# Performance work log

Measured on AMD Instinct MI355X. Metric: run time of the kernel, lower is better.

## Reference

```python
import math
import jax, jax.numpy as jnp
import numpy as np

B, N, T, C, H = 16, 307, 24, 128, 8
D = C // H
FACTOR = 5
S = min(FACTOR * int(np.ceil(np.log(T))), T)   # sample_k (U_part) = 20
U = S                                          # n_top u = 20


def _pos_emb(t_len, c):
    pos = jnp.arange(t_len, dtype=jnp.float32)[:, None]
    div = jnp.exp(jnp.arange(0, c, 2, dtype=jnp.float32) * (-math.log(10000.0) / c))
    pe = jnp.zeros((t_len, c), dtype=jnp.float32)
    pe = pe.at[:, 0::2].set(jnp.sin(pos * div))
    pe = pe.at[:, 1::2].set(jnp.cos(pos * div))
    return pe  # [T, C]


def _layernorm(x, g, b, eps=1e-5):
    m = x.mean(-1, keepdims=True)
    v = ((x - m) ** 2).mean(-1, keepdims=True)
    return (x - m) / jnp.sqrt(v + eps) * g + b


def _forward(query, time_encoder, index_sample,
             emb_minute, emb_hour, emb_weekday, emb_month, emb_year,
             Wq, Wk, Wv, Wo, bo, ff_w1, ff_b1, ff_w2, ff_b2,
             ln1_g, ln1_b, ln2_g, ln2_b):
    # DataEmbedding: x + positional + temporal (dropout = identity in eval)
    pe = _pos_emb(T, C)                                   # [T, C]
    te = (emb_minute[time_encoder[..., 0]] + emb_hour[time_encoder[..., 1]]
          + emb_weekday[time_encoder[..., 2]] + emb_month[time_encoder[..., 3]]
          + emb_year[time_encoder[..., 4]])               # [B, T, C]
    x = query + pe[None, None, :, :] + te[:, None, :, :]  # [B, N, T, C]

    # QKV projections -> [B, H, N, T, D]
    def proj(inp, W):
        return (inp @ W).reshape(B, N, T, H, D).transpose(0, 3, 1, 2, 4)
    Q, K, V = proj(x, Wq), proj(x, Wk), proj(x, Wv)

    # ProbSparse: sample S keys per query position
    K_samp = K[:, :, :, index_sample, :]                  # [B, H, N, T, S, D]
    QK_samp = jnp.einsum('bhntd,bhntsd->bhnts', Q, K_samp)
    M = QK_samp.max(-1) - QK_samp.sum(-1) / S             # [B, H, N, T]
    _, M_top = jax.lax.top_k(M, U)                        # [B, H, N, U]

    Q_red = jnp.take_along_axis(Q, M_top[..., None], axis=3)  # [B, H, N, U, D]
    scores = jnp.einsum('bhnud,bhntd->bhnut', Q_red, K) * (1.0 / math.sqrt(D))
    attn = jax.nn.softmax(scores, axis=-1)
    upd = jnp.einsum('bhnut,bhntd->bhnud', attn, V)       # [B, H, N, U, D]

    # initial context = mean over T, then scatter-update top-u query rows
    ctx = jnp.broadcast_to(V.mean(axis=3, keepdims=True), V.shape)
    ctx = ctx.at[jnp.arange(B)[:, None, None, None],
                 jnp.arange(H)[None, :, None, None],
                 jnp.arange(N)[None, None, :, None],
                 M_top].set(upd)

    ctx = ctx.transpose(0, 2, 3, 1, 4).reshape(B, N, T, C)
    att_out = ctx @ Wo + bo

    x1 = _layernorm(att_out + x, ln1_g, ln1_b)
    ff = jax.nn.relu(x1 @ ff_w1 + ff_b1) @ ff_w2 + ff_b2
    out = _layernorm(ff + x1, ln2_g, ln2_b)
    return out


def setup_inputs() -> dict:
    key = jax.random.key(0)
    ks = jax.random.split(key, 32)
    def nrm(i, shape, s=0.02):
        return jax.random.normal(ks[i], shape, dtype=jnp.float32) * s
    inp = {
        'value': jax.random.normal(ks[0], (B, N, T, C), dtype=jnp.float32),
        'key_in': jax.random.normal(ks[1], (B, N, T, C), dtype=jnp.float32),
        'query': jax.random.normal(ks[2], (B, N, T, C), dtype=jnp.float32),
        't': 1,
        'time_encoder': jax.random.randint(ks[3], (B, T, 5), 0, 10),
        'index_sample': jax.random.randint(ks[4], (T, S), 0, T),
        'emb_minute': nrm(5, (70, C), 1.0), 'emb_hour': nrm(6, (30, C), 1.0),
        'emb_weekday': nrm(7, (10, C), 1.0), 'emb_month': nrm(8, (40, C), 1.0),
        'emb_year': nrm(9, (400, C), 1.0),
        'Wq': nrm(10, (C, C)), 'Wk': nrm(11, (C, C)), 'Wv': nrm(12, (C, C)),
        'Wo': nrm(13, (C, C)), 'bo': jnp.zeros((C,), jnp.float32),
        'ff_w1': nrm(14, (C, 4 * C)), 'ff_b1': jnp.zeros((4 * C,), jnp.float32),
        'ff_w2': nrm(15, (4 * C, C)), 'ff_b2': jnp.zeros((C,), jnp.float32),
        'ln1_g': jnp.ones((C,), jnp.float32), 'ln1_b': jnp.zeros((C,), jnp.float32),
        'ln2_g': jnp.ones((C,), jnp.float32), 'ln2_b': jnp.zeros((C,), jnp.float32),
    }
    return inp


def reference(value, key_in, query, t, time_encoder, index_sample,
              emb_minute, emb_hour, emb_weekday, emb_month, emb_year,
              Wq, Wk, Wv, Wo, bo, ff_w1, ff_b1, ff_w2, ff_b2,
              ln1_g, ln1_b, ln2_g, ln2_b):
    # value, key_in, t are accepted but unused, matching the torch module
    return _forward(query, time_encoder, index_sample,
                    emb_minute, emb_hour, emb_weekday, emb_month, emb_year,
                    Wq, Wk, Wv, Wo, bo, ff_w1, ff_b1, ff_w2, ff_b2,
                    ln1_g, ln1_b, ln2_g, ln2_b)
```

## Files before the change

### kernel.cpp

```cpp
#include <hip/hip_runtime.h>
#include <hip/hip_bf16.h>
#include <cmath>

namespace {
constexpr int B_ = 16, N_ = 307, T_ = 24, C_ = 128, H_ = 8, D_ = 16, S_ = 20, U_ = 20;
constexpr int NROW = B_ * N_ * T_;
constexpr int NX = NROW * C_;
constexpr int TEPE_N = B_ * T_ * C_;
constexpr int FF = 4 * C_;
constexpr int BM = 32;
constexpr int NBLK_MM = NROW / BM;
constexpr int BMF = 64;
constexpr int NBLK_FF = NROW / BMF;
constexpr int NUNIT = B_ * H_ * N_;
}

typedef __attribute__((ext_vector_type(8))) short short8;
typedef __attribute__((ext_vector_type(4))) short short4_;
typedef __attribute__((ext_vector_type(4))) float f32x4;

__device__ inline short f2bf(float v) {
    union { float f; unsigned u; } a; a.f = v;
    unsigned r = a.u + 0x7fff + ((a.u >> 16) & 1);
    return (short)(r >> 16);
}
__device__ inline float bf2f(short s) {
    return __bfloat162float(*(const __hip_bfloat16*)&s);
}

__global__ void k_tepe(const int* __restrict__ te,
                       const float* __restrict__ e_min, const float* __restrict__ e_hr,
                       const float* __restrict__ e_wd, const float* __restrict__ e_mo,
                       const float* __restrict__ e_yr, float* __restrict__ tepe,
                       const int* __restrict__ idxs, unsigned char* __restrict__ cntg) {
    int i = blockIdx.x * blockDim.x + threadIdx.x;
    if (i < TEPE_N) {
        int c = i & (C_ - 1);
        int bt = i >> 7;
        int t = bt % T_;
        const int* enc = te + bt * 5;
        float v = e_min[enc[0] * C_ + c] + e_hr[enc[1] * C_ + c] + e_wd[enc[2] * C_ + c]
                + e_mo[enc[3] * C_ + c] + e_yr[enc[4] * C_ + c];
        float ang = (float)t * expf(-(float)(c & ~1) * (9.210340371976184f / 128.0f));
        v += (c & 1) ? cosf(ang) : sinf(ang);
        tepe[i] = v;
    }
    if (blockIdx.x == 0) {
        __shared__ int scnt[T_ * 32];
        for (int j = threadIdx.x; j < T_ * 32; j += 256) scnt[j] = 0;
        __syncthreads();
        for (int j = threadIdx.x; j < T_ * S_; j += 256) {
            int t = j / S_;
            atomicAdd(&scnt[t * 32 + idxs[j]], 1);
        }
        __syncthreads();
        for (int j = threadIdx.x; j < 192; j += 256) {
            unsigned v = (unsigned)scnt[4 * j] | ((unsigned)scnt[4 * j + 1] << 8)
                       | ((unsigned)scnt[4 * j + 2] << 16) | ((unsigned)scnt[4 * j + 3] << 24);
            ((unsigned*)cntg)[j] = v;
        }
    }
}

__global__ void k_xprep(const float* __restrict__ query, const float* __restrict__ tepe,
                        short* __restrict__ xbf) {
    int i = blockIdx.x * 256 + threadIdx.x;
    int c4 = i & 31;
    int gr = i >> 5;
    int t = gr % T_;
    int b = gr / (N_ * T_);
    float4 q = *(const float4*)(query + 4 * (size_t)i);
    float4 p = *(const float4*)(tepe + (size_t)(b * T_ + t) * C_ + c4 * 4);
    short4_ s;
    s.x = f2bf(q.x + p.x); s.y = f2bf(q.y + p.y);
    s.z = f2bf(q.z + p.z); s.w = f2bf(q.w + p.w);
    *(short4_*)&xbf[4 * (size_t)i] = s;
}

__global__ void k_wcvt_qkv(const float* __restrict__ Wq, const float* __restrict__ Wk,
                           const float* __restrict__ Wv, short* __restrict__ wqkvf) {
    int i = blockIdx.x * 256 + threadIdx.x;
    int tile = i >> 9, l = (i >> 3) & 63, e = i & 7;
    int c_tile = tile >> 2, ks = tile & 3;
    int c_all = c_tile * 16 + (l & 15);
    int k = ks * 32 + (l >> 4) * 8 + e;
    int m = c_all >> 7, c = c_all & (C_ - 1);
    const float* W = (m == 0) ? Wq : (m == 1) ? Wk : Wv;
    wqkvf[i] = f2bf(W[k * C_ + c]);
}

__global__ void k_wcvt2(const float* __restrict__ w1, const float* __restrict__ w2,
                        const float* __restrict__ Wo,
                        short* __restrict__ w1f, short* __restrict__ w2f,
                        short* __restrict__ wof) {
    int i = blockIdx.x * 256 + threadIdx.x;
    if (i < C_ * FF) {
        int tile = i >> 9, l = (i >> 3) & 63, e = i & 7;
        int jtile = tile >> 2, ks = tile & 3;
        int j = jtile * 16 + (l & 15);
        int k = ks * 32 + (l >> 4) * 8 + e;
        w1f[i] = f2bf(w1[k * FF + j]);
    } else if (i < 2 * C_ * FF) {
        int i2 = i - C_ * FF;
        int tile = i2 >> 9, l = (i2 >> 3) & 63, e = i2 & 7;
        int c_tile = tile >> 4, ks = tile & 15;
        int c = c_tile * 16 + (l & 15);
        int j = ks * 32 + (l >> 4) * 8 + e;
        w2f[i2] = f2bf(w2[j * C_ + c]);
    } else {
        int i3 = i - 2 * C_ * FF;
        int tile = i3 >> 9, l = (i3 >> 3) & 63, e = i3 & 7;
        int c_tile = tile >> 2, ks = tile & 3;
        int c = c_tile * 16 + (l & 15);
        int k = ks * 32 + (l >> 4) * 8 + e;
        wof[i3] = f2bf(Wo[k * C_ + c]);
    }
}

__global__ __launch_bounds__(256) void k_qkv_mfma(
    const short* __restrict__ xbf, const short* __restrict__ wqkvf,
    short* __restrict__ Q, short* __restrict__ K, short* __restrict__ V) {
    __shared__ __align__(16) short xs[BM * C_];
    int tid = threadIdx.x;
    int r0 = blockIdx.x * BM;
    {
        int row = tid >> 3;
        int cb = (tid & 7) * 16;
        const short* src = xbf + (size_t)(r0 + row) * C_ + cb;
        short8 v0 = *(const short8*)(src);
        short8 v1 = *(const short8*)(src + 8);
        *(short8*)&xs[(row * C_ + cb) ^ ((row & 7) << 3)] = v0;
        *(short8*)&xs[(row * C_ + cb + 8) ^ ((row & 7) << 3)] = v1;
    }
    __syncthreads();
    int w = tid >> 6, l = tid & 63;
    int lr = l & 15, lk = l >> 4;
    int swz = (lr & 7) << 3;
    short8 bx[2][4];
#pragma unroll
    for (int rt = 0; rt < 2; rt++)
#pragma unroll
        for (int ks = 0; ks < 4; ks++)
            bx[rt][ks] = *(const short8*)&xs[((rt * 16 + lr) * C_ + ks * 32 + lk * 8) ^ swz];
    size_t base[2];
#pragma unroll
    for (int rt = 0; rt < 2; rt++) {
        int gr = r0 + rt * 16 + lr;
        int t = gr % T_;
        int n = (gr / T_) % N_;
        int b = gr / (N_ * T_);
        base[rt] = ((size_t)b * H_ * N_ + n) * (T_ * D_) + t * D_;
    }
#pragma unroll
    for (int jt = 0; jt < 6; jt++) {
        int ctile = w * 6 + jt;
        const short* ap = wqkvf + (size_t)ctile * 2048 + l * 8;
        short8 acur[4];
#pragma unroll
        for (int ks = 0; ks < 4; ks++) acur[ks] = *(const short8*)(ap + ks * 512);
        f32x4 acc[2] = {{0.f, 0.f, 0.f, 0.f}, {0.f, 0.f, 0.f, 0.f}};
#pragma unroll
        for (int ks = 0; ks < 4; ks++) {
#pragma unroll
            for (int rt = 0; rt < 2; rt++)
                acc[rt] = __builtin_amdgcn_mfma_f32_16x16x32_bf16(acur[ks], bx[rt][ks], acc[rt], 0, 0, 0);
        }
        int c0 = ctile * 16 + lk * 4;
        int m = c0 >> 7;
        int c = c0 & (C_ - 1);
        int h = c >> 4, d = c & 15;
        short* dst = (m == 0) ? Q : (m == 1) ? K : V;
#pragma unroll
        for (int rt = 0; rt < 2; rt++) {
            short4_ sv;
            sv.x = f2bf(acc[rt][0]); sv.y = f2bf(acc[rt][1]);
            sv.z = f2bf(acc[rt][2]); sv.w = f2bf(acc[rt][3]);
            *(short4_*)&dst[base[rt] + (size_t)h * (N_ * T_ * D_) + d] = sv;
        }
    }
}

__global__ __launch_bounds__(256) void k_attn(
    const short* __restrict__ Q, const short* __restrict__ K, const short* __restrict__ V,
    const unsigned char* __restrict__ cntg, short* __restrict__ ctx) {
    __shared__ __align__(16) short Qbf[4][32 * 24], Kbf[4][32 * 24];
    __shared__ __align__(16) short Vt[4][16 * 40];
    __shared__ __align__(16) short Pbf[4][32 * 40];
    __shared__ unsigned char cntS[T_ * 32];
    __shared__ float Mv[4][T_];
    __shared__ int keepS[4][T_];
    __shared__ float meanVs[4][D_];
    int tid = threadIdx.x;
    int wid = tid >> 6, l = tid & 63;
    int e = blockIdx.x * 4 + wid;
    const short* qb = Q + (size_t)e * (T_ * D_);
    const short* kb = K + (size_t)e * (T_ * D_);
    const short* vb = V + (size_t)e * (T_ * D_);
    if (l < 48) {
        int t = l >> 1, hf = l & 1;
        *(short8*)&Qbf[wid][t * 24 + hf * 8] = *(const short8*)(qb + t * 16 + hf * 8);
        *(short8*)&Kbf[wid][t * 24 + hf * 8] = *(const short8*)(kb + t * 16 + hf * 8);
    }
    for (int i = l; i < 96; i += 64) {
        int t = i >> 2, c4 = i & 3;
        short4_ v = *(const short4_*)(vb + t * 16 + c4 * 4);
        Vt[wid][(c4 * 4 + 0) * 40 + t] = v.x;
        Vt[wid][(c4 * 4 + 1) * 40 + t] = v.y;
        Vt[wid][(c4 * 4 + 2) * 40 + t] = v.z;
        Vt[wid][(c4 * 4 + 3) * 40 + t] = v.w;
    }
    for (int i = l; i < 128; i += 64) {
        int d = i >> 3, c = 24 + (i & 7);
        Vt[wid][d * 40 + c] = 0;
    }
    if (tid < 192) ((int*)cntS)[tid] = ((const int*)cntg)[tid];
    __syncthreads();
    if (l >= 48) {
        int d = l - 48;
        float s = 0.f;
        for (int t = 0; t < T_; t++) s += bf2f(Vt[wid][d * 40 + t]);
        meanVs[wid][d] = s * (1.0f / T_);
    }
    int lr = l & 15, lk = l >> 4;
    short8 zz = {};
    short8 kf0 = zz, kf1 = zz, qf0 = zz, qf1 = zz;
    if (lk < 2) {
        kf0 = *(const short8*)&Kbf[wid][lr * 24 + lk * 8];
        kf1 = *(const short8*)&Kbf[wid][(16 + lr) * 24 + lk * 8];
        qf0 = *(const short8*)&Qbf[wid][lr * 24 + lk * 8];
        qf1 = *(const short8*)&Qbf[wid][(16 + lr) * 24 + lk * 8];
    }
    f32x4 zf = {0.f, 0.f, 0.f, 0.f};
    f32x4 s00 = __builtin_amdgcn_mfma_f32_16x16x32_bf16(kf0, qf0, zf, 0, 0, 0);
    f32x4 s01 = __builtin_amdgcn_mfma_f32_16x16x32_bf16(kf1, qf0, zf, 0, 0, 0);
    f32x4 s10 = __builtin_amdgcn_mfma_f32_16x16x32_bf16(kf0, qf1, zf, 0, 0, 0);
    f32x4 s11 = __builtin_amdgcn_mfma_f32_16x16x32_bf16(kf1, qf1, zf, 0, 0, 0);
#pragma unroll
    for (int rt = 0; rt < 2; rt++) {
        int t = rt * 16 + lr;
        int tt = (t < T_) ? t : 0;
        f32x4 c0 = rt ? s10 : s00;
        f32x4 c1 = rt ? s11 : s01;
        float mx = -1e30f, sm = 0.f;
#pragma unroll
        for (int i = 0; i < 4; i++) {
            int cA = cntS[tt * 32 + lk * 4 + i];
            if (cA) { mx = fmaxf(mx, c0[i]); sm += (float)cA * c0[i]; }
        }
        if (lk < 2) {
#pragma unroll
            for (int i = 0; i < 4; i++) {
                int cB = cntS[tt * 32 + 16 + lk * 4 + i];
                if (cB) { mx = fmaxf(mx, c1[i]); sm += (float)cB * c1[i]; }
            }
        }
        mx = fmaxf(mx, __shfl_xor(mx, 16));
        mx = fmaxf(mx, __shfl_xor(mx, 32));
        sm += __shfl_xor(sm, 16);
        sm += __shfl_xor(sm, 32);
        if (lk == 0 && t < T_) Mv[wid][t] = mx - sm * (1.0f / S_);
    }
    __syncthreads();
    if (l < T_) {
        float mt = Mv[wid][l];
        int cnt2 = 0;
        for (int t2 = 0; t2 < T_; t2++) {
            float m2 = Mv[wid][t2];
            cnt2 += (m2 > mt) || (m2 == mt && t2 < l);
        }
        keepS[wid][l] = (cnt2 < U_) ? 1 : 0;
    }
#pragma unroll
    for (int rt = 0; rt < 2; rt++) {
        f32x4 c0 = rt ? s10 : s00;
        f32x4 c1 = rt ? s11 : s01;
        float lm = fmaxf(fmaxf(c0[0], c0[1]), fmaxf(c0[2], c0[3]));
        if (lk < 2) lm = fmaxf(lm, fmaxf(fmaxf(c1[0], c1[1]), fmaxf(c1[2], c1[3])));
        lm = fmaxf(lm, __shfl_xor(lm, 16));
        lm = fmaxf(lm, __shfl_xor(lm, 32));
        float e0[4], e1[4];
        float ls = 0.f;
#pragma unroll
        for (int i = 0; i < 4; i++) { e0[i] = __expf(0.25f * (c0[i] - lm)); ls += e0[i]; }
#pragma unroll
        for (int i = 0; i < 4; i++) { e1[i] = (lk < 2) ? __expf(0.25f * (c1[i] - lm)) : 0.f; ls += e1[i]; }
        ls += __shfl_xor(ls, 16);
        ls += __shfl_xor(ls, 32);
        float inv = 1.0f / ls;
        short4_ w0, w1;
        w0.x = f2bf(e0[0] * inv); w0.y = f2bf(e0[1] * inv);
        w0.z = f2bf(e0[2] * inv); w0.w = f2bf(e0[3] * inv);
        w1.x = f2bf(e1[0] * inv); w1.y = f2bf(e1[1] * inv);
        w1.z = f2bf(e1[2] * inv); w1.w = f2bf(e1[3] * inv);
        int trow = rt * 16 + lr;
        *(short4_*)&Pbf[wid][trow * 40 + lk * 4] = w0;
        *(short4_*)&Pbf[wid][trow * 40 + 16 + lk * 4] = w1;
    }
    __syncthreads();
    short8 vf = *(const short8*)&Vt[wid][lr * 40 + lk * 8];
    short8 pf0 = *(const short8*)&Pbf[wid][lr * 40 + lk * 8];
    short8 pf1 = *(const short8*)&Pbf[wid][(16 + lr) * 40 + lk * 8];
    f32x4 u0 = __builtin_amdgcn_mfma_f32_16x16x32_bf16(vf, pf0, zf, 0, 0, 0);
    f32x4 u1 = __builtin_amdgcn_mfma_f32_16x16x32_bf16(vf, pf1, zf, 0, 0, 0);
    int b = e / (H_ * N_);
    int h = (e / N_) % H_;
    int n = e % N_;
    float4 mv4 = *(const float4*)&meanVs[wid][lk * 4];
#pragma unroll
    for (int rt = 0; rt < 2; rt++) {
        int t = rt * 16 + lr;
        if (t < T_) {
            f32x4 u = rt ? u1 : u0;
            float4 o;
            if (keepS[wid][t]) { o.x = u[0]; o.y = u[1]; o.z = u[2]; o.w = u[3]; }
            else o = mv4;
            short4_ sv;
            sv.x = f2bf(o.x); sv.y = f2bf(o.y); sv.z = f2bf(o.z); sv.w = f2bf(o.w);
            *(short4_*)&ctx[((size_t)(b * N_ + n) * T_ + t) * C_ + h * D_ + lk * 4] = sv;
        }
    }
}

__global__ __launch_bounds__(256) void k_out_ln_mfma(
    const short* __restrict__ ctx, const short* __restrict__ wof, const float* __restrict__ bo,
    const float* __restrict__ query, const float* __restrict__ tepe,
    const float* __restrict__ g1, const float* __restrict__ b1,
    float* __restrict__ x1) {
    __shared__ __align__(16) short cbf[BM * C_];
    __shared__ __align__(16) float xf[BM][132];
    int tid = threadIdx.x;
    int r0 = blockIdx.x * BM;
    {
        int row = tid >> 3;
        int cb = (tid & 7) * 16;
        int gr = r0 + row;
        int t = gr % T_;
        int b = gr / (N_ * T_);
        const short* src = ctx + (size_t)gr * C_ + cb;
        const float* qsrc = query + (size_t)gr * C_ + cb;
        const float* tsrc = tepe + (size_t)(b * T_ + t) * C_ + cb;
        short8 v0 = *(const short8*)(src);
        short8 v1 = *(const short8*)(src + 8);
        int swz0 = (row & 7) << 3;
        *(short8*)&cbf[(row * C_ + cb) ^ swz0] = v0;
        *(short8*)&cbf[(row * C_ + cb + 8) ^ swz0] = v1;
#pragma unroll
        for (int i = 0; i < 4; i++) {
            float4 q4 = *(const float4*)(qsrc + 4 * i);
            float4 t4 = *(const float4*)(tsrc + 4 * i);
            float4 xr;
            xr.x = q4.x + t4.x; xr.y = q4.y + t4.y;
            xr.z = q4.z + t4.z; xr.w = q4.w + t4.w;
            *(float4*)&xf[row][cb + 4 * i] = xr;
        }
    }
    __syncthreads();
    int w = tid >> 6, l = tid & 63;
    int lr = l & 15, lk = l >> 4;
    int swz = (lr & 7) << 3;
    short8 bc[2][4];
#pragma unroll
    for (int rt = 0; rt < 2; rt++)
#pragma unroll
        for (int ks = 0; ks < 4; ks++)
            bc[rt][ks] = *(const short8*)&cbf[((rt * 16 + lr) * C_ + ks * 32 + lk * 8) ^ swz];
#pragma unroll
    for (int ct = 0; ct < 2; ct++) {
        int c_tile = w * 2 + ct;
        const short* ap = wof + (size_t)c_tile * 2048 + l * 8;
        short8 acur[4];
#pragma unroll
        for (int ks = 0; ks < 4; ks++) acur[ks] = *(const short8*)(ap + ks * 512);
        f32x4 acc[2] = {{0.f, 0.f, 0.f, 0.f}, {0.f, 0.f, 0.f, 0.f}};
#pragma unroll
        for (int ks = 0; ks < 4; ks++) {
#pragma unroll
            for (int rt = 0; rt < 2; rt++)
                acc[rt] = __builtin_amdgcn_mfma_f32_16x16x32_bf16(acur[ks], bc[rt][ks], acc[rt], 0, 0, 0);
        }
        int cc = c_tile * 16 + lk * 4;
        float4 bias = *(const float4*)(bo + cc);
#pragma unroll
        for (int rt = 0; rt < 2; rt++) {
            int rrow = rt * 16 + lr;
            float4 res = *(const float4*)&xf[rrow][cc];
            float4 o;
            o.x = acc[rt][0] + bias.x + res.x;
            o.y = acc[rt][1] + bias.y + res.y;
            o.z = acc[rt][2] + bias.z + res.z;
            o.w = acc[rt][3] + bias.w + res.w;
            *(float4*)&xf[rrow][cc] = o;
        }
    }
    __syncthreads();
    {
        int r = tid >> 3;
        int q = tid & 7;
        int cb = q * 16;
        float vals[16];
        float s = 0.f;
#pragma unroll
        for (int i = 0; i < 16; i++) { vals[i] = xf[r][cb + i]; s += vals[i]; }
        s += __shfl_xor(s, 1, 8);
        s += __shfl_xor(s, 2, 8);
        s += __shfl_xor(s, 4, 8);
        float mean = s * (1.f / C_);
        float vv = 0.f;
#pragma unroll
        for (int i = 0; i < 16; i++) { float d = vals[i] - mean; vv += d * d; }
        vv += __shfl_xor(vv, 1, 8);
        vv += __shfl_xor(vv, 2, 8);
        vv += __shfl_xor(vv, 4, 8);
        float rstd = rsqrtf(vv * (1.f / C_) + 1e-5f);
        float* op = x1 + (size_t)(r0 + r) * C_ + cb;
#pragma unroll
        for (int i4 = 0; i4 < 4; i4++) {
            float4 gv = *(const float4*)(g1 + cb + 4 * i4);
            float4 bv = *(const float4*)(b1 + cb + 4 * i4);
            float4 ov;
            ov.x = (vals[4 * i4 + 0] - mean) * rstd * gv.x + bv.x;
            ov.y = (vals[4 * i4 + 1] - mean) * rstd * gv.y + bv.y;
            ov.z = (vals[4 * i4 + 2] - mean) * rstd * gv.z + bv.z;
            ov.w = (vals[4 * i4 + 3] - mean) * rstd * gv.w + bv.w;
            *(float4*)(op + 4 * i4) = ov;
        }
    }
}

__global__ __launch_bounds__(512, 4) void k_ff_mfma(
    const float* __restrict__ x1, const short* __restrict__ w1f, const float* __restrict__ b1f,
    const short* __restrict__ w2f, const float* __restrict__ b2f,
    const float* __restrict__ g2, const float* __restrict__ b2ln,
    float* __restrict__ out) {
    __shared__ __align__(16) short xbf[BMF * C_];
    __shared__ __align__(16) short hbf[BMF * FF];
    float (*yf)[132] = (float(*)[132])hbf;
    int tid = threadIdx.x;
    int r0 = blockIdx.x * BMF;
    {
        int row = tid >> 3;
        int cb = (tid & 7) * 16;
        const float* src = x1 + (size_t)(r0 + row) * C_ + cb;
#pragma unroll
        for (int i = 0; i < 4; i++) {
            float4 v = *(const float4*)(src + 4 * i);
            short4_ sv;
            sv.x = f2bf(v.x); sv.y = f2bf(v.y); sv.z = f2bf(v.z); sv.w = f2bf(v.w);
            *(short4_*)&xbf[(row * C_ + cb + 4 * i) ^ ((row & 7) << 3)] = sv;
        }
    }
    __syncthreads();
    int w = tid >> 6, l = tid & 63;
    int lr = l & 15, lk = l >> 4;
    int swz = (lr & 7) << 3;
    {
        short8 bx[4][4];
#pragma unroll
        for (int rt = 0; rt < 4; rt++)
#pragma unroll
            for (int ks = 0; ks < 4; ks++)
                bx[rt][ks] = *(const short8*)&xbf[((rt * 16 + lr) * C_ + ks * 32 + lk * 8) ^ swz];
#pragma unroll
        for (int jt = 0; jt < 4; jt++) {
            int jtile = w * 4 + jt;
            const short* ap = w1f + (size_t)jtile * 2048 + l * 8;
            short8 acur[4];
#pragma unroll
            for (int ks = 0; ks < 4; ks++) acur[ks] = *(const short8*)(ap + ks * 512);
            f32x4 acc[4] = {{0.f, 0.f, 0.f, 0.f}, {0.f, 0.f, 0.f, 0.f},
                            {0.f, 0.f, 0.f, 0.f}, {0.f, 0.f, 0.f, 0.f}};
#pragma unroll
            for (int ks = 0; ks < 4; ks++) {
#pragma unroll
                for (int rt = 0; rt < 4; rt++)
                    acc[rt] = __builtin_amdgcn_mfma_f32_16x16x32_bf16(acur[ks], bx[rt][ks], acc[rt], 0, 0, 0);
            }
            int j0 = jtile * 16 + lk * 4;
            float4 bias = *(const float4*)(b1f + j0);
#pragma unroll
            for (int rt = 0; rt < 4; rt++) {
                int rr = rt * 16 + lr;
                short4_ hv;
                hv.x = f2bf(fmaxf(acc[rt][0] + bias.x, 0.f));
                hv.y = f2bf(fmaxf(acc[rt][1] + bias.y, 0.f));
                hv.z = f2bf(fmaxf(acc[rt][2] + bias.z, 0.f));
                hv.w = f2bf(fmaxf(acc[rt][3] + bias.w, 0.f));
                *(short4_*)&hbf[(rr * FF + j0) ^ swz] = hv;
            }
        }
    }
    __syncthreads();
    f32x4 acc2[4] = {{0.f, 0.f, 0.f, 0.f}, {0.f, 0.f, 0.f, 0.f},
                     {0.f, 0.f, 0.f, 0.f}, {0.f, 0.f, 0.f, 0.f}};
    int ctile = w;
#pragma unroll 4
    for (int ks = 0; ks < 16; ks++) {
        short8 aw = *(const short8*)(w2f + ((size_t)(ctile * 16 + ks)) * 512 + l * 8);
#pragma unroll
        for (int rt = 0; rt < 4; rt++) {
            short8 hx = *(const short8*)&hbf[((rt * 16 + lr) * FF + ks * 32 + lk * 8) ^ swz];
            acc2[rt] = __builtin_amdgcn_mfma_f32_16x16x32_bf16(aw, hx, acc2[rt], 0, 0, 0);
        }
    }
    int cc = ctile * 16 + lk * 4;
    float4 bias2 = *(const float4*)(b2f + cc);
    float4 res[4];
#pragma unroll
    for (int rt = 0; rt < 4; rt++)
        res[rt] = *(const float4*)(x1 + (size_t)(r0 + rt * 16 + lr) * C_ + cc);
    __syncthreads();
#pragma unroll
    for (int rt = 0; rt < 4; rt++) {
        float4 o;
        o.x = acc2[rt][0] + bias2.x + res[rt].x;
        o.y = acc2[rt][1] + bias2.y + res[rt].y;
        o.z = acc2[rt][2] + bias2.z + res[rt].z;
        o.w = acc2[rt][3] + bias2.w + res[rt].w;
        *(float4*)&yf[rt * 16 + lr][cc] = o;
    }
    __syncthreads();
    {
        int r = tid >> 3;
        int q = tid & 7;
        int cb = q * 16;
        float vals[16];
        float s = 0.f;
#pragma unroll
        for (int i = 0; i < 16; i++) { vals[i] = yf[r][cb + i]; s += vals[i]; }
        s += __shfl_xor(s, 1, 8);
        s += __shfl_xor(s, 2, 8);
        s += __shfl_xor(s, 4, 8);
        float mean = s * (1.f / C_);
        float vv = 0.f;
#pragma unroll
        for (int i = 0; i < 16; i++) { float d = vals[i] - mean; vv += d * d; }
        vv += __shfl_xor(vv, 1, 8);
        vv += __shfl_xor(vv, 2, 8);
        vv += __shfl_xor(vv, 4, 8);
        float rstd = rsqrtf(vv * (1.f / C_) + 1e-5f);
        float* op = out + (size_t)(r0 + r) * C_ + cb;
#pragma unroll
        for (int i4 = 0; i4 < 4; i4++) {
            float4 gv = *(const float4*)(g2 + cb + 4 * i4);
            float4 bv = *(const float4*)(b2ln + cb + 4 * i4);
            float4 ov;
            ov.x = (vals[4 * i4 + 0] - mean) * rstd * gv.x + bv.x;
            ov.y = (vals[4 * i4 + 1] - mean) * rstd * gv.y + bv.y;
            ov.z = (vals[4 * i4 + 2] - mean) * rstd * gv.z + bv.z;
            ov.w = (vals[4 * i4 + 3] - mean) * rstd * gv.w + bv.w;
            *(float4*)(op + 4 * i4) = ov;
        }
    }
}

extern "C" void kernel_launch(void* const* d_in, const int* in_sizes, int n_in,
                              void* d_out, int out_size, void* d_ws, size_t ws_size,
                              hipStream_t stream) {
    const float* query = (const float*)d_in[2];
    const int* time_enc = (const int*)d_in[4];
    const int* index_sample = (const int*)d_in[5];
    const float* e_min = (const float*)d_in[6];
    const float* e_hr  = (const float*)d_in[7];
    const float* e_wd  = (const float*)d_in[8];
    const float* e_mo  = (const float*)d_in[9];
    const float* e_yr  = (const float*)d_in[10];
    const float* Wq = (const float*)d_in[11];
    const float* Wk = (const float*)d_in[12];
    const float* Wv = (const float*)d_in[13];
    const float* Wo = (const float*)d_in[14];
    const float* bo = (const float*)d_in[15];
    const float* ffw1 = (const float*)d_in[16];
    const float* ffb1 = (const float*)d_in[17];
    const float* ffw2 = (const float*)d_in[18];
    const float* ffb2 = (const float*)d_in[19];
    const float* ln1g = (const float*)d_in[20];
    const float* ln1b = (const float*)d_in[21];
    const float* ln2g = (const float*)d_in[22];
    const float* ln2b = (const float*)d_in[23];

    float* ws = (float*)d_ws;
    float* tepe = ws;
    float* region1 = ws + TEPE_N;
    float* region2 = region1 + NX;
    float* region3 = region2 + NX;
    float* region4 = region3 + NX;

    short* Qb = (short*)region1;
    short* Kb = (short*)region2;
    short* Vb = (short*)region3;
    short* ctxb = (short*)region4;
    float* x1 = region1;

    short* xbf = (short*)region4;
    short* wqkvf = (short*)region4 + NX;
    unsigned char* cntg = (unsigned char*)((short*)region4 + NX + 49152);
    short* w1f = (short*)region2;
    short* w2f = w1f + C_ * FF;
    short* wof = w2f + C_ * FF;

    k_tepe<<<dim3(TEPE_N / 256), dim3(256), 0, stream>>>(
        time_enc, e_min, e_hr, e_wd, e_mo, e_yr, tepe, index_sample, cntg);
    k_xprep<<<dim3(NX / 4 / 256), dim3(256), 0, stream>>>(query, tepe, xbf);
    k_wcvt_qkv<<<dim3(384 * C_ / 256), dim3(256), 0, stream>>>(Wq, Wk, Wv, wqkvf);
    k_qkv_mfma<<<dim3(NBLK_MM), dim3(256), 0, stream>>>(xbf, wqkvf, Qb, Kb, Vb);
    k_attn<<<dim3(NUNIT / 4), dim3(256), 0, stream>>>(
        Qb, Kb, Vb, cntg, ctxb);
    k_wcvt2<<<dim3((2 * C_ * FF + C_ * C_) / 256), dim3(256), 0, stream>>>(
        ffw1, ffw2, Wo, w1f, w2f, wof);
    k_out_ln_mfma<<<dim3(NBLK_MM), dim3(256), 0, stream>>>(
        ctxb, wof, bo, query, tepe, ln1g, ln1b, x1);
    k_ff_mfma<<<dim3(NBLK_FF), dim3(512), 0, stream>>>(
        x1, w1f, ffb1, w2f, ffb2, ln2g, ln2b, (float*)d_out);
}
```

Measured before the change: 199.6 us.

## Fuse input prep into QKV GEMM and merge output projection with FFN tail

Removes the standalone x-prep kernel by computing query+embedding and bf16 conversion directly in the QKV GEMM staging. Merges the output-projection+LayerNorm1 kernel with the feed-forward+LayerNorm2 kernel, keeping the LN1 result in shared memory as bf16 rather than writing and re-reading fp32 x1 from global memory. This cuts global memory traffic and launches, at the cost of a larger shared-memory footprint per block and a bf16-rounded residual for the second LayerNorm.

```diff
diff --git a/kernel.cpp b/kernel.cpp
--- a/kernel.cpp
+++ b/kernel.cpp
@@ -10,8 +10,8 @@
 constexpr int FF = 4 * C_;
 constexpr int BM = 32;
 constexpr int NBLK_MM = NROW / BM;
-constexpr int BMF = 64;
-constexpr int NBLK_FF = NROW / BMF;
+constexpr int BMT = 64;
+constexpr int NBLK_T = NROW / BMT;
 constexpr int NUNIT = B_ * H_ * N_;
 }
 
@@ -60,21 +60,6 @@
             ((unsigned*)cntg)[j] = v;
         }
     }
-}
-
-__global__ void k_xprep(const float* __restrict__ query, const float* __restrict__ tepe,
-                        short* __restrict__ xbf) {
-    int i = blockIdx.x * 256 + threadIdx.x;
-    int c4 = i & 31;
-    int gr = i >> 5;
-    int t = gr % T_;
-    int b = gr / (N_ * T_);
-    float4 q = *(const float4*)(query + 4 * (size_t)i);
-    float4 p = *(const float4*)(tepe + (size_t)(b * T_ + t) * C_ + c4 * 4);
-    short4_ s;
-    s.x = f2bf(q.x + p.x); s.y = f2bf(q.y + p.y);
-    s.z = f2bf(q.z + p.z); s.w = f2bf(q.w + p.w);
-    *(short4_*)&xbf[4 * (size_t)i] = s;
 }
 
 __global__ void k_wcvt_qkv(const float* __restrict__ Wq, const float* __restrict__ Wk,
@@ -118,7 +103,8 @@
 }
 
 __global__ __launch_bounds__(256) void k_qkv_mfma(
-    const short* __restrict__ xbf, const short* __restrict__ wqkvf,
+    const float* __restrict__ query, const float* __restrict__ tepe,
+    const short* __restrict__ wqkvf,
     short* __restrict__ Q, short* __restrict__ K, short* __restrict__ V) {
     __shared__ __align__(16) short xs[BM * C_];
     int tid = threadIdx.x;
@@ -126,11 +112,21 @@
     {
         int row = tid >> 3;
         int cb = (tid & 7) * 16;
-        const short* src = xbf + (size_t)(r0 + row) * C_ + cb;
-        short8 v0 = *(const short8*)(src);
-        short8 v1 = *(const short8*)(src + 8);
-        *(short8*)&xs[(row * C_ + cb) ^ ((row & 7) << 3)] = v0;
-        *(short8*)&xs[(row * C_ + cb + 8) ^ ((row & 7) << 3)] = v1;
+        int gr = r0 + row;
+        int t = gr % T_;
+        int b = gr / (N_ * T_);
+        const float* qsrc = query + (size_t)gr * C_ + cb;
+        const float* tsrc = tepe + (size_t)(b * T_ + t) * C_ + cb;
+        int swz0 = (row & 7) << 3;
+#pragma unroll
+        for (int i = 0; i < 4; i++) {
+            float4 q4 = *(const float4*)(qsrc + 4 * i);
+            float4 t4 = *(const float4*)(tsrc + 4 * i);
+            short4_ sv;
+            sv.x = f2bf(q4.x + t4.x); sv.y = f2bf(q4.y + t4.y);
+            sv.z = f2bf(q4.z + t4.z); sv.w = f2bf(q4.w + t4.w);
+            *(short4_*)&xs[(row * C_ + cb + 4 * i) ^ swz0] = sv;
+        }
     }
     __syncthreads();
     int w = tid >> 6, l = tid & 63;
@@ -321,29 +317,34 @@
     }
 }
 
-__global__ __launch_bounds__(256) void k_out_ln_mfma(
+__global__ __launch_bounds__(512, 4) void k_tail(
     const short* __restrict__ ctx, const short* __restrict__ wof, const float* __restrict__ bo,
     const float* __restrict__ query, const float* __restrict__ tepe,
     const float* __restrict__ g1, const float* __restrict__ b1,
-    float* __restrict__ x1) {
-    __shared__ __align__(16) short cbf[BM * C_];
-    __shared__ __align__(16) float xf[BM][132];
+    const short* __restrict__ w1f, const float* __restrict__ b1f,
+    const short* __restrict__ w2f, const float* __restrict__ b2f,
+    const float* __restrict__ g2, const float* __restrict__ b2ln,
+    float* __restrict__ out) {
+    __shared__ __align__(16) char smem[81920];
+    short* cbf = (short*)smem;
+    float (*xf)[132] = (float(*)[132])(smem + 16384);
+    short* x1bf = (short*)(smem + 65536);
+    short* hbf = (short*)smem;
+    float (*yf)[132] = (float(*)[132])smem;
     int tid = threadIdx.x;
-    int r0 = blockIdx.x * BM;
+    int r0 = blockIdx.x * BMT;
     {
         int row = tid >> 3;
         int cb = (tid & 7) * 16;
         int gr = r0 + row;
         int t = gr % T_;
         int b = gr / (N_ * T_);
-        const short* src = ctx + (size_t)gr * C_ + cb;
+        const short* csrc = ctx + (size_t)gr * C_ + cb;
         const float* qsrc = query + (size_t)gr * C_ + cb;
         const float* tsrc = tepe + (size_t)(b * T_ + t) * C_ + cb;
-        short8 v0 = *(const short8*)(src);
-        short8 v1 = *(const short8*)(src + 8);
         int swz0 = (row & 7) << 3;
-        *(short8*)&cbf[(row * C_ + cb) ^ swz0] = v0;
-        *(short8*)&cbf[(row * C_ + cb + 8) ^ swz0] = v1;
+        *(short8*)&cbf[(row * C_ + cb) ^ swz0] = *(const short8*)csrc;
+        *(short8*)&cbf[(row * C_ + cb + 8) ^ swz0] = *(const short8*)(csrc + 8);
 #pragma unroll
         for (int i = 0; i < 4; i++) {
             float4 q4 = *(const float4*)(qsrc + 4 * i);
@@ -358,38 +359,31 @@
     int w = tid >> 6, l = tid & 63;
     int lr = l & 15, lk = l >> 4;
     int swz = (lr & 7) << 3;
-    short8 bc[2][4];
-#pragma unroll
-    for (int rt = 0; rt < 2; rt++)
-#pragma unroll
-        for (int ks = 0; ks < 4; ks++)
-            bc[rt][ks] = *(const short8*)&cbf[((rt * 16 + lr) * C_ + ks * 32 + lk * 8) ^ swz];
-#pragma unroll
-    for (int ct = 0; ct < 2; ct++) {
-        int c_tile = w * 2 + ct;
-        const short* ap = wof + (size_t)c_tile * 2048 + l * 8;
-        short8 acur[4];
-#pragma unroll
-        for (int ks = 0; ks < 4; ks++) acur[ks] = *(const short8*)(ap + ks * 512);
-        f32x4 acc[2] = {{0.f, 0.f, 0.f, 0.f}, {0.f, 0.f, 0.f, 0.f}};
+    {
+        const short* ap = wof + (size_t)w * 2048 + l * 8;
+        f32x4 acc[4] = {{0.f, 0.f, 0.f, 0.f}, {0.f, 0.f, 0.f, 0.f},
+                        {0.f, 0.f, 0.f, 0.f}, {0.f, 0.f, 0.f, 0.f}};
 #pragma unroll
         for (int ks = 0; ks < 4; ks++) {
-#pragma unroll
-            for (int rt = 0; rt < 2; rt++)
-                acc[rt] = __builtin_amdgcn_mfma_f32_16x16x32_bf16(acur[ks], bc[rt][ks], acc[rt], 0, 0, 0);
-        }
-        int cc = c_tile * 16 + lk * 4;
+            short8 aw = *(const short8*)(ap + ks * 512);
+#pragma unroll
+            for (int rt = 0; rt < 4; rt++) {
+                short8 bc = *(const short8*)&cbf[((rt * 16 + lr) * C_ + ks * 32 + lk * 8) ^ swz];
+                acc[rt] = __builtin_amdgcn_mfma_f32_16x16x32_bf16(aw, bc, acc[rt], 0, 0, 0);
+            }
+        }
+        int cc = w * 16 + lk * 4;
         float4 bias = *(const float4*)(bo + cc);
 #pragma unroll
-        for (int rt = 0; rt < 2; rt++) {
-            int rrow = rt * 16 + lr;
-            float4 res = *(const float4*)&xf[rrow][cc];
+        for (int rt = 0; rt < 4; rt++) {
+            int rr = rt * 16 + lr;
+            float4 res = *(const float4*)&xf[rr][cc];
             float4 o;
             o.x = acc[rt][0] + bias.x + res.x;
             o.y = acc[rt][1] + bias.y + res.y;
             o.z = acc[rt][2] + bias.z + res.z;
             o.w = acc[rt][3] + bias.w + res.w;
-            *(float4*)&xf[rrow][cc] = o;
+            *(float4*)&xf[rr][cc] = o;
         }
     }
     __syncthreads();
@@ -412,54 +406,24 @@
         vv += __shfl_xor(vv, 2, 8);
         vv += __shfl_xor(vv, 4, 8);
         float rstd = rsqrtf(vv * (1.f / C_) + 1e-5f);
-        float* op = x1 + (size_t)(r0 + r) * C_ + cb;
-#pragma unroll
-        for (int i4 = 0; i4 < 4; i4++) {
-            float4 gv = *(const float4*)(g1 + cb + 4 * i4);
-            float4 bv = *(const float4*)(b1 + cb + 4 * i4);
-            float4 ov;
-            ov.x = (vals[4 * i4 + 0] - mean) * rstd * gv.x + bv.x;
-            ov.y = (vals[4 * i4 + 1] - mean) * rstd * gv.y + bv.y;
-            ov.z = (vals[4 * i4 + 2] - mean) * rstd * gv.z + bv.z;
-            ov.w = (vals[4 * i4 + 3] - mean) * rstd * gv.w + bv.w;
-            *(float4*)(op + 4 * i4) = ov;
-        }
-    }
-}
-
-__global__ __launch_bounds__(512, 4) void k_ff_mfma(
-    const float* __restrict__ x1, const short* __restrict__ w1f, const float* __restrict__ b1f,
-    const short* __restrict__ w2f, const float* __restrict__ b2f,
-    const float* __restrict__ g2, const float* __restrict__ b2ln,
-    float* __restrict__ out) {
-    __shared__ __align__(16) short xbf[BMF * C_];
-    __shared__ __align__(16) short hbf[BMF * FF];
-    float (*yf)[132] = (float(*)[132])hbf;
-    int tid = threadIdx.x;
-    int r0 = blockIdx.x * BMF;
-    {
-        int row = tid >> 3;
-        int cb = (tid & 7) * 16;
-        const float* src = x1 + (size_t)(r0 + row) * C_ + cb;
-#pragma unroll
-        for (int i = 0; i < 4; i++) {
-            float4 v = *(const float4*)(src + 4 * i);
-            short4_ sv;
-            sv.x = f2bf(v.x); sv.y = f2bf(v.y); sv.z = f2bf(v.z); sv.w = f2bf(v.w);
-            *(short4_*)&xbf[(row * C_ + cb + 4 * i) ^ ((row & 7) << 3)] = sv;
-        }
-    }
-    __syncthreads();
-    int w = tid >> 6, l = tid & 63;
-    int lr = l & 15, lk = l >> 4;
-    int swz = (lr & 7) << 3;
+        short8 o0, o1;
+#pragma unroll
+        for (int i = 0; i < 8; i++) {
+            o0[i] = f2bf((vals[i] - mean) * rstd * g1[cb + i] + b1[cb + i]);
+            o1[i] = f2bf((vals[8 + i] - mean) * rstd * g1[cb + 8 + i] + b1[cb + 8 + i]);
+        }
+        int swz0 = (r & 7) << 3;
+        *(short8*)&x1bf[(r * C_ + cb) ^ swz0] = o0;
+        *(short8*)&x1bf[(r * C_ + cb + 8) ^ swz0] = o1;
+    }
+    __syncthreads();
     {
         short8 bx[4][4];
 #pragma unroll
         for (int rt = 0; rt < 4; rt++)
 #pragma unroll
             for (int ks = 0; ks < 4; ks++)
-                bx[rt][ks] = *(const short8*)&xbf[((rt * 16 + lr) * C_ + ks * 32 + lk * 8) ^ swz];
+                bx[rt][ks] = *(const short8*)&x1bf[((rt * 16 + lr) * C_ + ks * 32 + lk * 8) ^ swz];
 #pragma unroll
         for (int jt = 0; jt < 4; jt++) {
             int jtile = w * 4 + jt;
@@ -492,22 +456,24 @@
     __syncthreads();
     f32x4 acc2[4] = {{0.f, 0.f, 0.f, 0.f}, {0.f, 0.f, 0.f, 0.f},
                      {0.f, 0.f, 0.f, 0.f}, {0.f, 0.f, 0.f, 0.f}};
-    int ctile = w;
 #pragma unroll 4
     for (int ks = 0; ks < 16; ks++) {
-        short8 aw = *(const short8*)(w2f + ((size_t)(ctile * 16 + ks)) * 512 + l * 8);
+        short8 aw = *(const short8*)(w2f + ((size_t)(w * 16 + ks)) * 512 + l * 8);
 #pragma unroll
         for (int rt = 0; rt < 4; rt++) {
             short8 hx = *(const short8*)&hbf[((rt * 16 + lr) * FF + ks * 32 + lk * 8) ^ swz];
             acc2[rt] = __builtin_amdgcn_mfma_f32_16x16x32_bf16(aw, hx, acc2[rt], 0, 0, 0);
         }
     }
-    int cc = ctile * 16 + lk * 4;
+    int cc = w * 16 + lk * 4;
     float4 bias2 = *(const float4*)(b2f + cc);
     float4 res[4];
 #pragma unroll
-    for (int rt = 0; rt < 4; rt++)
-        res[rt] = *(const float4*)(x1 + (size_t)(r0 + rt * 16 + lr) * C_ + cc);
+    for (int rt = 0; rt < 4; rt++) {
+        short4_ rb = *(const short4_*)&x1bf[((rt * 16 + lr) * C_ + cc) ^ swz];
+        res[rt].x = bf2f(rb.x); res[rt].y = bf2f(rb.y);
+        res[rt].z = bf2f(rb.z); res[rt].w = bf2f(rb.w);
+    }
     __syncthreads();
 #pragma unroll
     for (int rt = 0; rt < 4; rt++) {
@@ -589,9 +555,6 @@
     short* Kb = (short*)region2;
     short* Vb = (short*)region3;
     short* ctxb = (short*)region4;
-    float* x1 = region1;
-
-    short* xbf = (short*)region4;
     short* wqkvf = (short*)region4 + NX;
     unsigned char* cntg = (unsigned char*)((short*)region4 + NX + 49152);
     short* w1f = (short*)region2;
@@ -600,15 +563,14 @@
 
     k_tepe<<<dim3(TEPE_N / 256), dim3(256), 0, stream>>>(
         time_enc, e_min, e_hr, e_wd, e_mo, e_yr, tepe, index_sample, cntg);
-    k_xprep<<<dim3(NX / 4 / 256), dim3(256), 0, stream>>>(query, tepe, xbf);
     k_wcvt_qkv<<<dim3(384 * C_ / 256), dim3(256), 0, stream>>>(Wq, Wk, Wv, wqkvf);
-    k_qkv_mfma<<<dim3(NBLK_MM), dim3(256), 0, stream>>>(xbf, wqkvf, Qb, Kb, Vb);
+    k_qkv_mfma<<<dim3(NBLK_MM), dim3(256), 0, stream>>>(
+        query, tepe, wqkvf, Qb, Kb, Vb);
     k_attn<<<dim3(NUNIT / 4), dim3(256), 0, stream>>>(
         Qb, Kb, Vb, cntg, ctxb);
     k_wcvt2<<<dim3((2 * C_ * FF + C_ * C_) / 256), dim3(256), 0, stream>>>(
         ffw1, ffw2, Wo, w1f, w2f, wof);
-    k_out_ln_mfma<<<dim3(NBLK_MM), dim3(256), 0, stream>>>(
-        ctxb, wof, bo, query, tepe, ln1g, ln1b, x1);
-    k_ff_mfma<<<dim3(NBLK_FF), dim3(512), 0, stream>>>(
-        x1, w1f, ffb1, w2f, ffb2, ln2g, ln2b, (float*)d_out);
-}
+    k_tail<<<dim3(NBLK_T), dim3(512), 0, stream>>>(
+        ctxb, wof, bo, query, tepe, ln1g, ln1b,
+        w1f, ffb1, w2f, ffb2, ln2g, ln2b, (float*)d_out);
+}
```

Result: faster. 170.6 us (-14.5%).
